# Kernel optimization log

Measured on AMD Instinct MI355X. Metric: run time of the kernel, lower is better.

The kernel has to match this reference:

```python
import jax, jax.numpy as jnp
import numpy as np


def setup_inputs() -> dict:
    key = jax.random.key(0)
    ks = jax.random.split(key, 6)
    N, E, C_in, C_out, C_e = 50000, 800000, 64, 64, 1
    x = jax.random.normal(ks[0], (N, C_in), dtype=jnp.float32)
    edge_index = jax.random.randint(ks[1], (2, E), 0, N, dtype=jnp.int64)
    edge_attr = jax.random.uniform(ks[2], (E, C_e), dtype=jnp.float32)
    W_fc = jax.random.normal(ks[3], (C_out, C_in), dtype=jnp.float32) * (1.0 / np.sqrt(C_in))
    W_edge = jax.random.normal(ks[4], (C_e, C_e), dtype=jnp.float32) * (1.0 / np.sqrt(C_in))
    W_att = jax.random.normal(ks[5], (1, 2 * C_out + C_e), dtype=jnp.float32) * (1.0 / np.sqrt(C_in))
    return {"x": x, "edge_index": edge_index, "edge_attr": edge_attr,
            "W_fc": W_fc, "W_edge": W_edge, "W_att": W_att}


def reference(x, edge_index, edge_attr, W_fc, W_edge, W_att):
    # x: [N, C_in], edge_index: [2, E], edge_attr: [E, C_e]
    row, col = edge_index[0], edge_index[1]
    num_node = x.shape[0]
    xcol = x[col] @ W_fc.T            # [E, C_out] gather + linear
    xrow = x[row] @ W_fc.T            # [E, C_out]
    ed = edge_attr @ W_edge.T         # [E, C_e]
    alpha = jnp.concatenate([xrow, xcol, ed], axis=1) @ W_att.T  # [E, 1]
    alpha = jax.nn.leaky_relu(alpha, negative_slope=0.01)
    # Faithful to source: softmax over singleton dim=1 -> all ones.
    alpha = jax.nn.softmax(alpha, axis=1)
    h = alpha * xcol                  # [E, C_out]
    z = jax.ops.segment_sum(h, row, num_segments=num_node)  # scatter_sum over dst
    return z
```

## Files before the change

kernel.cpp:

```cpp
#include <hip/hip_runtime.h>
#include <hip/hip_bf16.h>


#define BSHIFT 6
#define BNODES 64
#define CAPB 2048
#define CAP 48
#define OVFCAP 128
#define SPILLCAP 65536
#define MAXNB 1024

__device__ inline unsigned short f2bf(float f) {
    __hip_bfloat16 h = __float2bfloat16(f);
    return *reinterpret_cast<unsigned short*>(&h);
}

__global__ void zero_kernel(int* __restrict__ a, int n) {
    int i = blockIdx.x * blockDim.x + threadIdx.x;
    int s = gridDim.x * blockDim.x;
    for (; i < n; i += s) a[i] = 0;
}

#define SMEM_BYTES (64 * 68 * 4 + 16 * 64 * 4)
__global__ __launch_bounds__(256) void fc_split(
        const float* __restrict__ x, const float* __restrict__ Wfc,
        unsigned short* __restrict__ y, int N,
        const int* __restrict__ eidx, unsigned* __restrict__ buckets,
        int* __restrict__ cursor, int* __restrict__ spillcnt, int* __restrict__ spill,
        int E, int NB, int splitB) {
    __shared__ __align__(16) char smem[SMEM_BYTES];
    if ((int)blockIdx.x < splitB) {
        int* hist  = (int*)smem;
        int* bases = hist + MAXNB;
        int chunk = (E + splitB - 1) / splitB;
        int e0 = (int)blockIdx.x * chunk;
        int e1 = e0 + chunk; if (e1 > E) e1 = E;
        int ea = (e0 + 3) & ~3;
        int eb = e1 & ~3;
        for (int i = threadIdx.x; i < NB; i += 256) hist[i] = 0;
        __syncthreads();
        if ((int)threadIdx.x < ea - e0) atomicAdd(&hist[eidx[e0 + threadIdx.x] >> BSHIFT], 1);
        {
            const int4* r4p = (const int4*)eidx;
            for (int i = (ea >> 2) + threadIdx.x; i < (eb >> 2); i += 256) {
                int4 v = r4p[i];
                atomicAdd(&hist[v.x >> BSHIFT], 1);
                atomicAdd(&hist[v.y >> BSHIFT], 1);
                atomicAdd(&hist[v.z >> BSHIFT], 1);
                atomicAdd(&hist[v.w >> BSHIFT], 1);
            }
        }
        if ((int)threadIdx.x < e1 - eb) atomicAdd(&hist[eidx[eb + threadIdx.x] >> BSHIFT], 1);
        __syncthreads();
        for (int b = threadIdx.x; b < NB; b += 256) {
            int c = hist[b];
            bases[b] = c ? atomicAdd(&cursor[b * 16], c) : 0;
            hist[b] = 0;
        }
        __syncthreads();
        const int4* r4p = (const int4*)eidx;
        const int4* c4p = (const int4*)(eidx + E);
        auto emit = [&](int r, int c) {
            int b = r >> BSHIFT;
            int pos = bases[b] + atomicAdd(&hist[b], 1);
            if (pos < CAPB) {
                buckets[(size_t)b * CAPB + pos] =
                    ((unsigned)(r & (BNODES - 1)) << 16) | (unsigned)c;
            } else {
                int q = atomicAdd(spillcnt, 1);
                if (q < SPILLCAP) { spill[2 * q] = r; spill[2 * q + 1] = c; }
            }
        };
        if ((int)threadIdx.x < ea - e0) {
            int e = e0 + threadIdx.x;
            emit(eidx[e], eidx[E + e]);
        }
        for (int i = (ea >> 2) + threadIdx.x; i < (eb >> 2); i += 256) {
            int4 rv = r4p[i];
            int4 cv = c4p[i];
            emit(rv.x, cv.x);
            emit(rv.y, cv.y);
            emit(rv.z, cv.z);
            emit(rv.w, cv.w);
        }
        if ((int)threadIdx.x < e1 - eb) {
            int e = eb + threadIdx.x;
            emit(eidx[e], eidx[E + e]);
        }
    } else {
        float (*sW)[68] = (float (*)[68])smem;
        float (*sX)[64] = (float (*)[64])(smem + 64 * 68 * 4);
        for (int i = threadIdx.x; i < 4096; i += 256) sW[i >> 6][i & 63] = Wfc[i];
        int row0 = ((int)blockIdx.x - splitB) << 4;
        for (int i = threadIdx.x; i < 1024; i += 256) {
            int r = i >> 6, k = i & 63, gr = row0 + r;
            sX[r][k] = (gr < N) ? x[(size_t)gr * 64 + k] : 0.f;
        }
        __syncthreads();
        int co = threadIdx.x & 63;
        int rq = threadIdx.x >> 6;
        const float4* wrow = reinterpret_cast<const float4*>(&sW[co][0]);
        const float4* xr0  = reinterpret_cast<const float4*>(&sX[4 * rq + 0][0]);
        const float4* xr1  = reinterpret_cast<const float4*>(&sX[4 * rq + 1][0]);
        const float4* xr2  = reinterpret_cast<const float4*>(&sX[4 * rq + 2][0]);
        const float4* xr3  = reinterpret_cast<const float4*>(&sX[4 * rq + 3][0]);
        float a0 = 0, a1 = 0, a2 = 0, a3 = 0;
#pragma unroll
        for (int m = 0; m < 16; ++m) {
            float4 w  = wrow[m];
            float4 v0 = xr0[m], v1 = xr1[m], v2 = xr2[m], v3 = xr3[m];
            a0 = fmaf(w.x, v0.x, fmaf(w.y, v0.y, fmaf(w.z, v0.z, fmaf(w.w, v0.w, a0))));
            a1 = fmaf(w.x, v1.x, fmaf(w.y, v1.y, fmaf(w.z, v1.z, fmaf(w.w, v1.w, a1))));
            a2 = fmaf(w.x, v2.x, fmaf(w.y, v2.y, fmaf(w.z, v2.z, fmaf(w.w, v2.w, a2))));
            a3 = fmaf(w.x, v3.x, fmaf(w.y, v3.y, fmaf(w.z, v3.z, fmaf(w.w, v3.w, a3))));
        }
        int g = row0 + 4 * rq;
        if (g + 3 < N) {
            y[(size_t)(g + 0) * 64 + co] = f2bf(a0);
            y[(size_t)(g + 1) * 64 + co] = f2bf(a1);
            y[(size_t)(g + 2) * 64 + co] = f2bf(a2);
            y[(size_t)(g + 3) * 64 + co] = f2bf(a3);
        } else {
            if (g + 0 < N) y[(size_t)(g + 0) * 64 + co] = f2bf(a0);
            if (g + 1 < N) y[(size_t)(g + 1) * 64 + co] = f2bf(a1);
            if (g + 2 < N) y[(size_t)(g + 2) * 64 + co] = f2bf(a2);
        }
    }
}

__device__ inline void acc_bf8(const uint2* yb, int c, int ch4,
                               float& r0, float& r1, float& r2, float& r3) {
    uint2 u = yb[(size_t)c * 16 + ch4];
    r0 += __uint_as_float(u.x << 16);
    r1 += __uint_as_float(u.x & 0xffff0000u);
    r2 += __uint_as_float(u.y << 16);
    r3 += __uint_as_float(u.y & 0xffff0000u);
}
__global__ __launch_bounds__(512) void gatherz2(
        const unsigned* __restrict__ buckets, const int* __restrict__ cursor,
        const uint2* __restrict__ yb2, float4* __restrict__ z4, int N,
        const int* __restrict__ spillcnt, const int* __restrict__ spill) {
    __shared__ int cntL[BNODES];
    __shared__ int slotsL[BNODES * CAP];
    __shared__ int ovfN[OVFCAP], ovfC[OVFCAP], ovfn_sh;
    int b  = (int)blockIdx.x;
    int lo = b << BSHIFT;
    for (int i = threadIdx.x; i < BNODES; i += 512) cntL[i] = 0;
    if (threadIdx.x == 0) ovfn_sh = 0;
    __syncthreads();
    int ecnt = cursor[b * 16]; if (ecnt > CAPB) ecnt = CAPB;
    const unsigned* blist = buckets + (size_t)b * CAPB;
    auto ingest = [&](unsigned e) {
        int n = (int)(e >> 16);
        int c = (int)(e & 0xffffu);
        int slot = atomicAdd(&cntL[n], 1);
        if (slot < CAP) slotsL[n * CAP + slot] = c;
        else { int q = atomicAdd(&ovfn_sh, 1);
               if (q < OVFCAP) { ovfN[q] = n; ovfC[q] = c; } }
    };
    {
        const uint4* blist4 = (const uint4*)blist;
        int n4 = ecnt >> 2;
        for (int p = threadIdx.x; p < n4; p += 512) {
            uint4 ee = blist4[p];
            ingest(ee.x); ingest(ee.y); ingest(ee.z); ingest(ee.w);
        }
        int base = n4 << 2;
        if ((int)threadIdx.x < ecnt - base) ingest(blist[base + threadIdx.x]);
    }
    int sc = *spillcnt;
    if (sc > SPILLCAP) sc = SPILLCAP;
    for (int i = threadIdx.x; i < sc; i += 512) {
        int r = spill[2 * i];
        if ((r >> BSHIFT) == b) {
            int n = r & (BNODES - 1), c = spill[2 * i + 1];
            int slot = atomicAdd(&cntL[n], 1);
            if (slot < CAP) slotsL[n * CAP + slot] = c;
            else { int q = atomicAdd(&ovfn_sh, 1);
                   if (q < OVFCAP) { ovfN[q] = n; ovfC[q] = c; } }
        }
    }
    __syncthreads();
    int on = ovfn_sh; if (on > OVFCAP) on = OVFCAP;
    int lane = threadIdx.x & 63;
    int wv   = threadIdx.x >> 6;
    int sub  = lane >> 4;
    int ch4  = lane & 15;
    for (int n = wv; n < BNODES; n += 8) {
        int node = lo + n;
        if (node >= N) break;
        int deg = cntL[n]; if (deg > CAP) deg = CAP;
        const int* srow = &slotsL[n * CAP];
        float A0=0,A1=0,A2=0,A3=0, B0=0,B1=0,B2=0,B3=0,
              C0=0,C1=0,C2=0,C3=0, D0=0,D1=0,D2=0,D3=0;
        for (int j = 0; j < deg; j += 16) {
            int j0 = j + sub, j1 = j + 4 + sub, j2 = j + 8 + sub, j3 = j + 12 + sub;
            int c0 = (j0 < deg) ? srow[j0] : -1;
            int c1 = (j1 < deg) ? srow[j1] : -1;
            int c2 = (j2 < deg) ? srow[j2] : -1;
            int c3 = (j3 < deg) ? srow[j3] : -1;
            if (c0 >= 0) acc_bf8(yb2, c0, ch4, A0, A1, A2, A3);
            if (c1 >= 0) acc_bf8(yb2, c1, ch4, B0, B1, B2, B3);
            if (c2 >= 0) acc_bf8(yb2, c2, ch4, C0, C1, C2, C3);
            if (c3 >= 0) acc_bf8(yb2, c3, ch4, D0, D1, D2, D3);
        }
        for (int k = 0; k < on; ++k)
            if (ovfN[k] == n && sub == 0)
                acc_bf8(yb2, ovfC[k], ch4, A0, A1, A2, A3);
        float r0 = (A0 + B0) + (C0 + D0);
        float r1 = (A1 + B1) + (C1 + D1);
        float r2 = (A2 + B2) + (C2 + D2);
        float r3 = (A3 + B3) + (C3 + D3);
        r0 += __shfl_xor(r0, 16, 64); r0 += __shfl_xor(r0, 32, 64);
        r1 += __shfl_xor(r1, 16, 64); r1 += __shfl_xor(r1, 32, 64);
        r2 += __shfl_xor(r2, 16, 64); r2 += __shfl_xor(r2, 32, 64);
        r3 += __shfl_xor(r3, 16, 64); r3 += __shfl_xor(r3, 32, 64);
        if (lane < 16)
            z4[(size_t)node * 16 + ch4] = make_float4(r0, r1, r2, r3);
    }
}

__global__ void fc_kernel(const float* __restrict__ x, const float* __restrict__ Wfc,
                          float* __restrict__ y, int N) {
    __shared__ float sW[64][65];
    __shared__ float sX[4][64];
    for (int i = threadIdx.x; i < 64 * 64; i += 256) sW[i >> 6][i & 63] = Wfc[i];
    int r = threadIdx.x >> 6, co = threadIdx.x & 63;
    int gRow = (blockIdx.x << 2) + r;
    sX[r][co] = (gRow < N) ? x[gRow * 64 + co] : 0.f;
    __syncthreads();
    if (gRow >= N) return;
    float acc = 0.f;
#pragma unroll
    for (int k = 0; k < 64; ++k) acc = fmaf(sX[r][k], sW[co][k], acc);
    y[gRow * 64 + co] = acc;
}
__global__ void scatter_kernel(const int* __restrict__ eidx, const float* __restrict__ y,
                               float* __restrict__ z, int E) {
    int lane = threadIdx.x & 63;
    int g  = (int)((blockIdx.x * blockDim.x + threadIdx.x) >> 6);
    int nG = (int)((gridDim.x * blockDim.x) >> 6);
    for (int e = g; e < E; e += nG) {
        int r = eidx[e], c = eidx[E + e];
        atomicAdd(&z[r * 64 + lane], y[c * 64 + lane]);
    }
}

extern "C" void kernel_launch(void* const* d_in, const int* in_sizes, int n_in,
                              void* d_out, int out_size, void* d_ws, size_t ws_size,
                              hipStream_t stream) {
    const float* x    = (const float*)d_in[0];
    const int*   eidx = (const int*)d_in[1];
    const float* Wfc  = (const float*)d_in[3];
    float*       z    = (float*)d_out;

    int N = in_sizes[0] / 64;
    int E = in_sizes[1] / 2;
    int NB = (N + BNODES - 1) >> BSHIFT;

    char* w = (char*)d_ws;
    size_t off = 0;
    int* cursor   = (int*)(w + off); off += (size_t)NB * 16 * sizeof(int);
    int* spillcnt = (int*)(w + off); off += sizeof(int);
    off = (off + 255) & ~(size_t)255;
    int* spill    = (int*)(w + off); off += (size_t)2 * SPILLCAP * sizeof(int);
    off = (off + 255) & ~(size_t)255;
    unsigned* buckets = (unsigned*)(w + off); off += (size_t)NB * CAPB * sizeof(unsigned);
    off = (off + 255) & ~(size_t)255;
    unsigned short* yb = (unsigned short*)(w + off); off += (size_t)N * 64 * sizeof(unsigned short);

    if (ws_size >= off && NB <= MAXNB && N <= 65536 && (E & 3) == 0) {
        zero_kernel<<<32, 256, 0, stream>>>(cursor, NB * 16 + 1);
        int splitB = 128;
        int fcB = (N + 15) / 16;
        fc_split<<<splitB + fcB, 256, 0, stream>>>(x, Wfc, yb, N, eidx, buckets,
                                                   cursor, spillcnt, spill, E, NB, splitB);
        gatherz2<<<NB, 512, 0, stream>>>(buckets, cursor, (const uint2*)yb,
                                         (float4*)z, N, spillcnt, spill);
    } else {
        float* y = (float*)d_ws;
        hipMemsetAsync(d_out, 0, (size_t)out_size * sizeof(float), stream);
        fc_kernel<<<(N + 3) / 4, 256, 0, stream>>>(x, Wfc, y, N);
        scatter_kernel<<<4096, 256, 0, stream>>>(eidx, y, z, E);
    }
}
```

Baseline: 56.46 us.

## Replace global-cursor bucketing with per-block private segments and counts

Result: slower. 64.30 us (+13.9%).

```diff
diff --git a/kernel.cpp b/kernel.cpp
--- a/kernel.cpp
+++ b/kernel.cpp
@@ -4,11 +4,12 @@
 
 #define BSHIFT 6
 #define BNODES 64
-#define CAPB 2048
+#define SCAP 32
 #define CAP 48
 #define OVFCAP 128
 #define SPILLCAP 65536
 #define MAXNB 1024
+#define SPLITB 128
 
 __device__ inline unsigned short f2bf(float f) {
     __hip_bfloat16 h = __float2bfloat16(f);
@@ -25,46 +26,26 @@
 __global__ __launch_bounds__(256) void fc_split(
         const float* __restrict__ x, const float* __restrict__ Wfc,
         unsigned short* __restrict__ y, int N,
-        const int* __restrict__ eidx, unsigned* __restrict__ buckets,
-        int* __restrict__ cursor, int* __restrict__ spillcnt, int* __restrict__ spill,
+        const int* __restrict__ eidx, unsigned* __restrict__ segs,
+        int* __restrict__ counts, int* __restrict__ spillcnt, int* __restrict__ spill,
         int E, int NB, int splitB) {
     __shared__ __align__(16) char smem[SMEM_BYTES];
     if ((int)blockIdx.x < splitB) {
-        int* hist  = (int*)smem;
-        int* bases = hist + MAXNB;
+        int* hist = (int*)smem;
+        int blk = (int)blockIdx.x;
         int chunk = (E + splitB - 1) / splitB;
-        int e0 = (int)blockIdx.x * chunk;
+        int e0 = blk * chunk;
         int e1 = e0 + chunk; if (e1 > E) e1 = E;
         int ea = (e0 + 3) & ~3;
         int eb = e1 & ~3;
         for (int i = threadIdx.x; i < NB; i += 256) hist[i] = 0;
         __syncthreads();
-        if ((int)threadIdx.x < ea - e0) atomicAdd(&hist[eidx[e0 + threadIdx.x] >> BSHIFT], 1);
-        {
-            const int4* r4p = (const int4*)eidx;
-            for (int i = (ea >> 2) + threadIdx.x; i < (eb >> 2); i += 256) {
-                int4 v = r4p[i];
-                atomicAdd(&hist[v.x >> BSHIFT], 1);
-                atomicAdd(&hist[v.y >> BSHIFT], 1);
-                atomicAdd(&hist[v.z >> BSHIFT], 1);
-                atomicAdd(&hist[v.w >> BSHIFT], 1);
-            }
-        }
-        if ((int)threadIdx.x < e1 - eb) atomicAdd(&hist[eidx[eb + threadIdx.x] >> BSHIFT], 1);
-        __syncthreads();
-        for (int b = threadIdx.x; b < NB; b += 256) {
-            int c = hist[b];
-            bases[b] = c ? atomicAdd(&cursor[b * 16], c) : 0;
-            hist[b] = 0;
-        }
-        __syncthreads();
-        const int4* r4p = (const int4*)eidx;
-        const int4* c4p = (const int4*)(eidx + E);
+        unsigned* myseg = segs + (size_t)blk * NB * SCAP;
         auto emit = [&](int r, int c) {
             int b = r >> BSHIFT;
-            int pos = bases[b] + atomicAdd(&hist[b], 1);
-            if (pos < CAPB) {
-                buckets[(size_t)b * CAPB + pos] =
+            int slot = atomicAdd(&hist[b], 1);
+            if (slot < SCAP) {
+                myseg[b * SCAP + slot] =
                     ((unsigned)(r & (BNODES - 1)) << 16) | (unsigned)c;
             } else {
                 int q = atomicAdd(spillcnt, 1);
@@ -75,6 +56,8 @@
             int e = e0 + threadIdx.x;
             emit(eidx[e], eidx[E + e]);
         }
+        const int4* r4p = (const int4*)eidx;
+        const int4* c4p = (const int4*)(eidx + E);
         for (int i = (ea >> 2) + threadIdx.x; i < (eb >> 2); i += 256) {
             int4 rv = r4p[i];
             int4 cv = c4p[i];
@@ -86,6 +69,11 @@
         if ((int)threadIdx.x < e1 - eb) {
             int e = eb + threadIdx.x;
             emit(eidx[e], eidx[E + e]);
+        }
+        __syncthreads();
+        for (int b = threadIdx.x; b < NB; b += 256) {
+            int c = hist[b];
+            counts[(size_t)blk * NB + b] = c > SCAP ? SCAP : c;
         }
     } else {
         float (*sW)[68] = (float (*)[68])smem;
@@ -137,9 +125,10 @@
     r3 += __uint_as_float(u.y & 0xffff0000u);
 }
 __global__ __launch_bounds__(512) void gatherz2(
-        const unsigned* __restrict__ buckets, const int* __restrict__ cursor,
+        const unsigned* __restrict__ segs, const int* __restrict__ counts,
         const uint2* __restrict__ yb2, float4* __restrict__ z4, int N,
-        const int* __restrict__ spillcnt, const int* __restrict__ spill) {
+        const int* __restrict__ spillcnt, const int* __restrict__ spill,
+        int NB, int splitB) {
     __shared__ int cntL[BNODES];
     __shared__ int slotsL[BNODES * CAP];
     __shared__ int ovfN[OVFCAP], ovfC[OVFCAP], ovfn_sh;
@@ -148,8 +137,8 @@
     for (int i = threadIdx.x; i < BNODES; i += 512) cntL[i] = 0;
     if (threadIdx.x == 0) ovfn_sh = 0;
     __syncthreads();
-    int ecnt = cursor[b * 16]; if (ecnt > CAPB) ecnt = CAPB;
-    const unsigned* blist = buckets + (size_t)b * CAPB;
+    int lane = threadIdx.x & 63;
+    int wv   = threadIdx.x >> 6;
     auto ingest = [&](unsigned e) {
         int n = (int)(e >> 16);
         int c = (int)(e & 0xffffu);
@@ -158,15 +147,10 @@
         else { int q = atomicAdd(&ovfn_sh, 1);
                if (q < OVFCAP) { ovfN[q] = n; ovfC[q] = c; } }
     };
-    {
-        const uint4* blist4 = (const uint4*)blist;
-        int n4 = ecnt >> 2;
-        for (int p = threadIdx.x; p < n4; p += 512) {
-            uint4 ee = blist4[p];
-            ingest(ee.x); ingest(ee.y); ingest(ee.z); ingest(ee.w);
-        }
-        int base = n4 << 2;
-        if ((int)threadIdx.x < ecnt - base) ingest(blist[base + threadIdx.x]);
+    for (int s = wv; s < splitB; s += 8) {
+        int cs = counts[(size_t)s * NB + b];
+        if (lane < cs)
+            ingest(segs[((size_t)s * NB + b) * SCAP + lane]);
     }
     int sc = *spillcnt;
     if (sc > SPILLCAP) sc = SPILLCAP;
@@ -182,8 +166,6 @@
     }
     __syncthreads();
     int on = ovfn_sh; if (on > OVFCAP) on = OVFCAP;
-    int lane = threadIdx.x & 63;
-    int wv   = threadIdx.x >> 6;
     int sub  = lane >> 4;
     int ch4  = lane & 15;
     for (int n = wv; n < BNODES; n += 8) {
@@ -260,23 +242,22 @@
 
     char* w = (char*)d_ws;
     size_t off = 0;
-    int* cursor   = (int*)(w + off); off += (size_t)NB * 16 * sizeof(int);
+    int* counts   = (int*)(w + off); off += (size_t)SPLITB * NB * sizeof(int);
     int* spillcnt = (int*)(w + off); off += sizeof(int);
     off = (off + 255) & ~(size_t)255;
     int* spill    = (int*)(w + off); off += (size_t)2 * SPILLCAP * sizeof(int);
     off = (off + 255) & ~(size_t)255;
-    unsigned* buckets = (unsigned*)(w + off); off += (size_t)NB * CAPB * sizeof(unsigned);
+    unsigned* segs = (unsigned*)(w + off); off += (size_t)SPLITB * NB * SCAP * sizeof(unsigned);
     off = (off + 255) & ~(size_t)255;
     unsigned short* yb = (unsigned short*)(w + off); off += (size_t)N * 64 * sizeof(unsigned short);
 
     if (ws_size >= off && NB <= MAXNB && N <= 65536 && (E & 3) == 0) {
-        zero_kernel<<<32, 256, 0, stream>>>(cursor, NB * 16 + 1);
-        int splitB = 128;
+        zero_kernel<<<1, 64, 0, stream>>>(spillcnt, 1);
         int fcB = (N + 15) / 16;
-        fc_split<<<splitB + fcB, 256, 0, stream>>>(x, Wfc, yb, N, eidx, buckets,
-                                                   cursor, spillcnt, spill, E, NB, splitB);
-        gatherz2<<<NB, 512, 0, stream>>>(buckets, cursor, (const uint2*)yb,
-                                         (float4*)z, N, spillcnt, spill);
+        fc_split<<<SPLITB + fcB, 256, 0, stream>>>(x, Wfc, yb, N, eidx, segs,
+                                                   counts, spillcnt, spill, E, NB, SPLITB);
+        gatherz2<<<NB, 512, 0, stream>>>(segs, counts, (const uint2*)yb,
+                                         (float4*)z, N, spillcnt, spill, NB, SPLITB);
     } else {
         float* y = (float*)d_ws;
         hipMemsetAsync(d_out, 0, (size_t)out_size * sizeof(float), stream);
```
